# Performance work log

Measured on AMD Instinct MI355X. Metric: run time of the kernel, lower is better.

Reference implementation:

```python
import jax, jax.numpy as jnp
import numpy as np

STRIDE = 2
PADDING = (1, 1)
OUT_PADDING = (0, 0)


def conv_transpose2d(x, weight, bias, stride, padding, out_padding):
    # weight: (Cin, Cout, kh, kw) -- torch ConvTranspose2d layout.
    # The original code does: stride-insert zeros, zero-pad by (k-1), append
    # out_padding rows/cols, valid-conv with the spatially-flipped kernel,
    # then crop `padding` from each side. That is exactly a dilated conv:
    kh, kw = weight.shape[2], weight.shape[3]
    w = jnp.flip(weight, (2, 3)).transpose(1, 0, 2, 3)  # (Cout, Cin, kh, kw)
    pad = ((kh - 1 - padding[0], kh - 1 - padding[0] + out_padding[0]),
           (kw - 1 - padding[1], kw - 1 - padding[1] + out_padding[1]))
    out = jax.lax.conv_general_dilated(
        x, w,
        window_strides=(1, 1),
        padding=pad,
        lhs_dilation=(stride, stride),
        dimension_numbers=('NCHW', 'OIHW', 'NCHW'))
    return out + bias[None, :, None, None]


def setup_inputs() -> dict:
    key = jax.random.key(0)
    k1, k2, k3 = jax.random.split(key, 3)
    Cin, Cout, kh, kw = 256, 128, 4, 4
    bnd = (1.0 / (Cin * kh * kw)) ** 0.5  # matches uniform_(-k**0.5, k**0.5)
    x = jax.random.normal(k1, (16, Cin, 64, 64), dtype=jnp.float32)
    weight = jax.random.uniform(k2, (Cin, Cout, kh, kw), jnp.float32, -bnd, bnd)
    bias = jax.random.uniform(k3, (Cout,), jnp.float32, -bnd, bnd)
    return {"x": x, "weight": weight, "bias": bias}


def reference(x, weight, bias):
    # Output: (16, 128, 128, 128) = (H-1)*2 - 2*1 + 4
    return conv_transpose2d(x, weight, bias, STRIDE, PADDING, OUT_PADDING)
```

## Files before the change

kernel.cpp:

```cpp
#include <hip/hip_runtime.h>
#include <stdint.h>

typedef unsigned short u16;
typedef __bf16 bf16x8 __attribute__((ext_vector_type(8)));
typedef float f32x4 __attribute__((ext_vector_type(4)));
typedef float f32x2 __attribute__((ext_vector_type(2)));

static const size_t XT_BYTES = (size_t)16 * 66 * 66 * 256 * 2;
static const size_t WK_BYTES = (size_t)2 * 2 * 8 * 2 * 2 * 128 * 32 * 2;

__device__ __forceinline__ u16 f2bf(float f) {
  unsigned u = __float_as_uint(f);
  unsigned r = (u + 0x7fff + ((u >> 16) & 1)) >> 16;
  return (u16)r;
}

__device__ __forceinline__ void ld_g2l16(const u16* g, void* l) {
  __builtin_amdgcn_global_load_lds(
      (const __attribute__((address_space(1))) unsigned int*)(uintptr_t)g,
      (__attribute__((address_space(3))) unsigned int*)(unsigned int)(uintptr_t)l,
      16, 0, 0);
}

__device__ __forceinline__ int swz4(int row) { return (row ^ (row >> 2)) & 3; }

__global__ __launch_bounds__(256) void prep_x(const float* __restrict__ x,
                                              u16* __restrict__ xt) {
  __shared__ __align__(16) u16 sh[64 * 264];
  const int t = threadIdx.x;
  const int ihp = blockIdx.x;
  const int n = blockIdx.y;
  u16* xtn = xt + ((size_t)(n * 66 + ihp)) * 66 * 256;
  if (ihp == 0 || ihp == 65) {
    for (int j = 0; j < 9; ++j) {
      int idx = j * 256 + t;
      if (idx < 2112) ((uint4*)xtn)[idx] = make_uint4(0, 0, 0, 0);
    }
    return;
  }
  const int ih = ihp - 1;
  const int iw0 = (t & 15) * 4;
  const int cb = (t >> 4) * 4;
  const int swz = (t & 3) << 3;
  const float* xb = x + (size_t)n * 1048576 + (size_t)ih * 64 + iw0;
#pragma unroll
  for (int it = 0; it < 4; ++it) {
    int ci0 = it * 64 + cb;
    float4 v0 = *(const float4*)(xb + (size_t)(ci0 + 0) * 4096);
    float4 v1 = *(const float4*)(xb + (size_t)(ci0 + 1) * 4096);
    float4 v2 = *(const float4*)(xb + (size_t)(ci0 + 2) * 4096);
    float4 v3 = *(const float4*)(xb + (size_t)(ci0 + 3) * 4096);
    int col = ci0 ^ swz;
    ushort4 u;
    u.x = f2bf(v0.x); u.y = f2bf(v1.x); u.z = f2bf(v2.x); u.w = f2bf(v3.x);
    *(ushort4*)&sh[(iw0 + 0) * 264 + col] = u;
    u.x = f2bf(v0.y); u.y = f2bf(v1.y); u.z = f2bf(v2.y); u.w = f2bf(v3.y);
    *(ushort4*)&sh[(iw0 + 1) * 264 + col] = u;
    u.x = f2bf(v0.z); u.y = f2bf(v1.z); u.z = f2bf(v2.z); u.w = f2bf(v3.z);
    *(ushort4*)&sh[(iw0 + 2) * 264 + col] = u;
    u.x = f2bf(v0.w); u.y = f2bf(v1.w); u.z = f2bf(v2.w); u.w = f2bf(v3.w);
    *(ushort4*)&sh[(iw0 + 3) * 264 + col] = u;
  }
  __syncthreads();
#pragma unroll
  for (int j = 0; j < 8; ++j) {
    int idx = j * 256 + t;
    int iw = idx >> 5;
    int chunk = idx & 31;
    uint4 v = *(const uint4*)&sh[iw * 264 + ((chunk ^ ((iw >> 2) & 3)) << 3)];
    *(uint4*)&xtn[(size_t)(iw + 1) * 256 + chunk * 8] = v;
  }
  if (t < 64) {
    int iwp = (t >> 5) * 65;
    int chunk = t & 31;
    *(uint4*)&xtn[(size_t)iwp * 256 + chunk * 8] = make_uint4(0, 0, 0, 0);
  }
}

__global__ __launch_bounds__(256) void prep_w(const float* __restrict__ w,
                                              u16* __restrict__ wk) {
  int id = blockIdx.x * 256 + threadIdx.x;
  int ci5 = id & 31;
  int co = (id >> 5) & 127;
  int q = (id >> 12) & 1;
  int dw = (id >> 13) & 1;
  int kc = (id >> 14) & 7;
  int dh = (id >> 17) & 1;
  int p = id >> 18;
  int ci = kc * 32 + ci5;
  int kh = 2 * dh + 1 - p;
  int kw = 2 * dw + 1 - q;
  wk[id] = f2bf(w[((ci * 128 + co) * 4 + kh) * 4 + kw]);
}

__global__ __launch_bounds__(256, 2) void gemm_ct(const u16* __restrict__ xt,
                                                  const u16* __restrict__ wk,
                                                  const float* __restrict__ bias,
                                                  float* __restrict__ out) {
  __shared__ __align__(16) u16 As[2][8192];
  __shared__ __align__(16) u16 Bs[2][4224];
  const int t = threadIdx.x;
  const int lane = t & 63;
  const int wv = t >> 6;
  const int wm = wv >> 1, wn = wv & 1;
  const int quad = lane >> 4, l15 = lane & 15;

  const int id = blockIdx.x;
  const int sid = (id & 7) * 128 + (id >> 3);
  const int mt = sid & 31;
  const int n = (sid >> 5) & 15;
  const int p = sid >> 9;
  const int m0 = mt * 2;

  const u16* wkp = wk + (size_t)p * 262144;
  const u16* xtn = xt + (size_t)n * (66 * 66 * 256);

  int aoffs[4];
#pragma unroll
  for (int it = 0; it < 4; ++it) {
    int c = it * 256 + t;
    int co = (c >> 2) & 127;
    aoffs[it] = (c >> 2) * 32 + ((c & 3) ^ swz4(co)) * 8;
  }
  int bsrc[3];
#pragma unroll
  for (int it = 0; it < 3; ++it) {
    int c = it * 256 + t;
    int r = (c >= 264) ? 1 : 0;
    int rem = c - 264 * r;
    int iwp = rem >> 2;
    bsrc[it] = r * 16896 + iwp * 256 + ((rem & 3) ^ swz4(iwp)) * 8;
  }

  int aro[2][4];
#pragma unroll
  for (int q = 0; q < 2; ++q)
#pragma unroll
    for (int i = 0; i < 4; ++i) {
      int co = wm * 64 + i * 16 + l15;
      aro[q][i] = (q * 128 + co) * 32 + (quad ^ swz4(co)) * 8;
    }
  int bro[3][4];
#pragma unroll
  for (int k = 0; k < 3; ++k)
#pragma unroll
    for (int j = 0; j < 4; ++j) {
      int b0 = j * 16 + l15 + k;
      bro[k][j] = wn * 2112 + b0 * 32 + (quad ^ swz4(b0)) * 8;
    }

  f32x4 acc[2][4][4];
#pragma unroll
  for (int q = 0; q < 2; ++q)
#pragma unroll
    for (int i = 0; i < 4; ++i)
#pragma unroll
      for (int j = 0; j < 4; ++j) acc[q][i][j] = (f32x4){0.f, 0.f, 0.f, 0.f};

  const int mpp1 = m0 + p + 1;

  auto stageA = [&](int buf, int s) {
    const u16* asrc = wkp + (size_t)s * 8192;
    u16* Ad = &As[buf][0];
#pragma unroll
    for (int it = 0; it < 4; ++it)
      ld_g2l16(asrc + aoffs[it], Ad + (it * 256 + t) * 8);
  };
  auto stageB = [&](int buf, int pr) {
    const int kc = pr & 7, dh = pr >> 3;
    const u16* bbase = xtn + (size_t)(mpp1 - dh) * 16896 + kc * 32;
    u16* Bd = &Bs[buf][0];
    ld_g2l16(bbase + bsrc[0], Bd + t * 8);
    ld_g2l16(bbase + bsrc[1], Bd + (256 + t) * 8);
    if (t < 16) ld_g2l16(bbase + bsrc[2], Bd + (512 + t) * 8);
  };

  stageA(0, 0);
  stageB(0, 0);
  asm volatile("s_waitcnt vmcnt(0)" ::: "memory");
  __builtin_amdgcn_s_barrier();
  asm volatile("" ::: "memory");

  bf16x8 keep[4];
#pragma unroll 1
  for (int pr = 0; pr < 16; ++pr) {
    const u16* Bc = &Bs[pr & 1][0];
    {
      stageA(1, 2 * pr + 1);
      __builtin_amdgcn_sched_barrier(0);
      if (pr < 15) stageB((pr + 1) & 1, pr + 1);
      __builtin_amdgcn_sched_barrier(0);
      const u16* Ac = &As[0][0];
      bf16x8 a0[4];
#pragma unroll
      for (int i = 0; i < 4; ++i) a0[i] = *(const bf16x8*)(Ac + aro[0][i]);
#pragma unroll
      for (int j = 0; j < 4; ++j) keep[j] = *(const bf16x8*)(Bc + bro[1][j]);
      __builtin_amdgcn_s_setprio(1);
#pragma unroll
      for (int i = 0; i < 4; ++i)
#pragma unroll
        for (int j = 0; j < 4; ++j)
          acc[0][i][j] = __builtin_amdgcn_mfma_f32_16x16x32_bf16(
              a0[i], keep[j], acc[0][i][j], 0, 0, 0);
      __builtin_amdgcn_s_setprio(0);
      bf16x8 a1[4], b2[4];
#pragma unroll
      for (int i = 0; i < 4; ++i) a1[i] = *(const bf16x8*)(Ac + aro[1][i]);
#pragma unroll
      for (int j = 0; j < 4; ++j) b2[j] = *(const bf16x8*)(Bc + bro[2][j]);
      __builtin_amdgcn_s_setprio(1);
#pragma unroll
      for (int i = 0; i < 4; ++i)
#pragma unroll
        for (int j = 0; j < 4; ++j)
          acc[1][i][j] = __builtin_amdgcn_mfma_f32_16x16x32_bf16(
              a1[i], b2[j], acc[1][i][j], 0, 0, 0);
      __builtin_amdgcn_s_setprio(0);
      if (pr < 15) {
        if (wv == 0)
          asm volatile("s_waitcnt lgkmcnt(0) vmcnt(3)" ::: "memory");
        else
          asm volatile("s_waitcnt lgkmcnt(0) vmcnt(2)" ::: "memory");
      } else {
        asm volatile("s_waitcnt lgkmcnt(0) vmcnt(0)" ::: "memory");
      }
      __builtin_amdgcn_s_barrier();
      asm volatile("" ::: "memory");
    }
    {
      if (pr < 15) stageA(0, 2 * pr + 2);
      __builtin_amdgcn_sched_barrier(0);
      const u16* Ac = &As[1][0];
      bf16x8 a0[4], b0[4];
#pragma unroll
      for (int i = 0; i < 4; ++i) a0[i] = *(const bf16x8*)(Ac + aro[0][i]);
#pragma unroll
      for (int j = 0; j < 4; ++j) b0[j] = *(const bf16x8*)(Bc + bro[0][j]);
      __builtin_amdgcn_s_setprio(1);
#pragma unroll
      for (int i = 0; i < 4; ++i)
#pragma unroll
        for (int j = 0; j < 4; ++j)
          acc[0][i][j] = __builtin_amdgcn_mfma_f32_16x16x32_bf16(
              a0[i], b0[j], acc[0][i][j], 0, 0, 0);
      __builtin_amdgcn_s_setprio(0);
      bf16x8 a1[4];
#pragma unroll
      for (int i = 0; i < 4; ++i) a1[i] = *(const bf16x8*)(Ac + aro[1][i]);
      __builtin_amdgcn_s_setprio(1);
#pragma unroll
      for (int i = 0; i < 4; ++i)
#pragma unroll
        for (int j = 0; j < 4; ++j)
          acc[1][i][j] = __builtin_amdgcn_mfma_f32_16x16x32_bf16(
              a1[i], keep[j], acc[1][i][j], 0, 0, 0);
      __builtin_amdgcn_s_setprio(0);
      asm volatile("s_waitcnt lgkmcnt(0) vmcnt(0)" ::: "memory");
      __builtin_amdgcn_s_barrier();
      asm volatile("" ::: "memory");
    }
  }

  const int oh = 2 * (m0 + wn) + p;
#pragma unroll
  for (int i = 0; i < 4; ++i) {
#pragma unroll
    for (int j = 0; j < 4; ++j) {
      int l = j * 16 + l15;
#pragma unroll
      for (int r = 0; r < 4; ++r) {
        int co = wm * 64 + i * 16 + quad * 4 + r;
        float bv = bias[co];
        f32x2 v;
        v.x = acc[0][i][j][r] + bv;
        v.y = acc[1][i][j][r] + bv;
        __builtin_nontemporal_store(
            v, (f32x2*)&out[(((size_t)n * 128 + co) * 128 + oh) * 128 + 2 * l]);
      }
    }
  }
}

__global__ __launch_bounds__(256) void ct_fallback(const float* __restrict__ x,
                                                   const float* __restrict__ w,
                                                   const float* __restrict__ bias,
                                                   float* __restrict__ out) {
  size_t id = (size_t)blockIdx.x * 256 + threadIdx.x;
  if (id >= (size_t)16 * 128 * 128 * 128) return;
  int ow = (int)(id & 127), oh = (int)(id >> 7) & 127;
  int co = (int)(id >> 14) & 127, n = (int)(id >> 21);
  int pp = oh & 1, m = oh >> 1, qq = ow & 1, l = ow >> 1;
  float s = bias[co];
  for (int ci = 0; ci < 256; ++ci) {
    for (int dh = 0; dh < 2; ++dh) {
      int ih = m + pp - dh;
      if (ih < 0 || ih > 63) continue;
      int kh = 2 * dh + 1 - pp;
      for (int dw = 0; dw < 2; ++dw) {
        int iw = l + qq - dw;
        if (iw < 0 || iw > 63) continue;
        int kw = 2 * dw + 1 - qq;
        s += x[(((size_t)n * 256 + ci) * 64 + ih) * 64 + iw] *
             w[((ci * 128 + co) * 4 + kh) * 4 + kw];
      }
    }
  }
  out[id] = s;
}

extern "C" void kernel_launch(void* const* d_in, const int* in_sizes, int n_in,
                              void* d_out, int out_size, void* d_ws, size_t ws_size,
                              hipStream_t stream) {
  const float* x = (const float*)d_in[0];
  const float* w = (const float*)d_in[1];
  const float* bias = (const float*)d_in[2];
  float* out = (float*)d_out;
  if (ws_size >= XT_BYTES + WK_BYTES) {
    u16* xt = (u16*)d_ws;
    u16* wkb = (u16*)((char*)d_ws + XT_BYTES);
    hipLaunchKernelGGL(prep_x, dim3(66, 16), dim3(256), 0, stream, x, xt);
    hipLaunchKernelGGL(prep_w, dim3(2048), dim3(256), 0, stream, w, wkb);
    hipLaunchKernelGGL(gemm_ct, dim3(1024), dim3(256), 0, stream, xt, wkb, bias, out);
  } else {
    hipLaunchKernelGGL(ct_fallback, dim3(131072), dim3(256), 0, stream, x, w, bias, out);
  }
}
```

Baseline: 246.3 us.

## Load weight fragments directly from global to registers and merge prep kernels

The GEMM kernel stops staging the weight (A) tiles through LDS and has each wave load its bf16 weight fragments straight from global memory into registers. The loop is software-pipelined with the A loads interleaved between MFMA groups, and the wait/barrier points are cut from two to one per iteration. The two preprocessing kernels for x and w are merged into one launch, saving a kernel launch. The trade-off is more redundant global/L2 traffic for weights and more register pressure, in exchange for lower LDS use and fewer synchronisations.

```diff
diff --git a/kernel.cpp b/kernel.cpp
--- a/kernel.cpp
+++ b/kernel.cpp
@@ -24,12 +24,30 @@
 
 __device__ __forceinline__ int swz4(int row) { return (row ^ (row >> 2)) & 3; }
 
-__global__ __launch_bounds__(256) void prep_x(const float* __restrict__ x,
-                                              u16* __restrict__ xt) {
+__global__ __launch_bounds__(256) void prep_all(const float* __restrict__ x,
+                                                const float* __restrict__ w,
+                                                u16* __restrict__ xt,
+                                                u16* __restrict__ wk) {
   __shared__ __align__(16) u16 sh[64 * 264];
   const int t = threadIdx.x;
-  const int ihp = blockIdx.x;
-  const int n = blockIdx.y;
+  const int bx = blockIdx.x;
+  if (bx >= 1056) {
+    int id = (bx - 1056) * 256 + t;
+    int ci5 = id & 31;
+    int co = (id >> 5) & 127;
+    int q = (id >> 12) & 1;
+    int dw = (id >> 13) & 1;
+    int kc = (id >> 14) & 7;
+    int dh = (id >> 17) & 1;
+    int p = id >> 18;
+    int ci = kc * 32 + ci5;
+    int kh = 2 * dh + 1 - p;
+    int kw = 2 * dw + 1 - q;
+    wk[id] = f2bf(w[((ci * 128 + co) * 4 + kh) * 4 + kw]);
+    return;
+  }
+  const int n = bx / 66;
+  const int ihp = bx - n * 66;
   u16* xtn = xt + ((size_t)(n * 66 + ihp)) * 66 * 256;
   if (ihp == 0 || ihp == 65) {
     for (int j = 0; j < 9; ++j) {
@@ -77,27 +95,10 @@
   }
 }
 
-__global__ __launch_bounds__(256) void prep_w(const float* __restrict__ w,
-                                              u16* __restrict__ wk) {
-  int id = blockIdx.x * 256 + threadIdx.x;
-  int ci5 = id & 31;
-  int co = (id >> 5) & 127;
-  int q = (id >> 12) & 1;
-  int dw = (id >> 13) & 1;
-  int kc = (id >> 14) & 7;
-  int dh = (id >> 17) & 1;
-  int p = id >> 18;
-  int ci = kc * 32 + ci5;
-  int kh = 2 * dh + 1 - p;
-  int kw = 2 * dw + 1 - q;
-  wk[id] = f2bf(w[((ci * 128 + co) * 4 + kh) * 4 + kw]);
-}
-
 __global__ __launch_bounds__(256, 2) void gemm_ct(const u16* __restrict__ xt,
                                                   const u16* __restrict__ wk,
                                                   const float* __restrict__ bias,
                                                   float* __restrict__ out) {
-  __shared__ __align__(16) u16 As[2][8192];
   __shared__ __align__(16) u16 Bs[2][4224];
   const int t = threadIdx.x;
   const int lane = t & 63;
@@ -112,16 +113,9 @@
   const int p = sid >> 9;
   const int m0 = mt * 2;
 
-  const u16* wkp = wk + (size_t)p * 262144;
+  const u16* wka = wk + (size_t)p * 262144 + wm * 2048 + l15 * 32 + quad * 8;
   const u16* xtn = xt + (size_t)n * (66 * 66 * 256);
 
-  int aoffs[4];
-#pragma unroll
-  for (int it = 0; it < 4; ++it) {
-    int c = it * 256 + t;
-    int co = (c >> 2) & 127;
-    aoffs[it] = (c >> 2) * 32 + ((c & 3) ^ swz4(co)) * 8;
-  }
   int bsrc[3];
 #pragma unroll
   for (int it = 0; it < 3; ++it) {
@@ -132,14 +126,6 @@
     bsrc[it] = r * 16896 + iwp * 256 + ((rem & 3) ^ swz4(iwp)) * 8;
   }
 
-  int aro[2][4];
-#pragma unroll
-  for (int q = 0; q < 2; ++q)
-#pragma unroll
-    for (int i = 0; i < 4; ++i) {
-      int co = wm * 64 + i * 16 + l15;
-      aro[q][i] = (q * 128 + co) * 32 + (quad ^ swz4(co)) * 8;
-    }
   int bro[3][4];
 #pragma unroll
   for (int k = 0; k < 3; ++k)
@@ -159,13 +145,6 @@
 
   const int mpp1 = m0 + p + 1;
 
-  auto stageA = [&](int buf, int s) {
-    const u16* asrc = wkp + (size_t)s * 8192;
-    u16* Ad = &As[buf][0];
-#pragma unroll
-    for (int it = 0; it < 4; ++it)
-      ld_g2l16(asrc + aoffs[it], Ad + (it * 256 + t) * 8);
-  };
   auto stageB = [&](int buf, int pr) {
     const int kc = pr & 7, dh = pr >> 3;
     const u16* bbase = xtn + (size_t)(mpp1 - dh) * 16896 + kc * 32;
@@ -175,7 +154,22 @@
     if (t < 16) ld_g2l16(bbase + bsrc[2], Bd + (512 + t) * 8);
   };
 
-  stageA(0, 0);
+  bf16x8 aC[4], aN[4];
+  auto ldA = [&](bf16x8* a, int s, int q) {
+    const u16* b = wka + (size_t)s * 8192 + q * 4096;
+#pragma unroll
+    for (int i = 0; i < 4; ++i) a[i] = *(const bf16x8*)(b + i * 512);
+  };
+
+#define MFMA16(ACC, AF, BF)                                              \
+  do {                                                                   \
+    _Pragma("unroll") for (int i = 0; i < 4; ++i)                        \
+        _Pragma("unroll") for (int j = 0; j < 4; ++j)                    \
+        ACC[i][j] = __builtin_amdgcn_mfma_f32_16x16x32_bf16(             \
+            AF[i], BF[j], ACC[i][j], 0, 0, 0);                           \
+  } while (0)
+
+  ldA(aC, 0, 0);
   stageB(0, 0);
   asm volatile("s_waitcnt vmcnt(0)" ::: "memory");
   __builtin_amdgcn_s_barrier();
@@ -185,82 +179,47 @@
 #pragma unroll 1
   for (int pr = 0; pr < 16; ++pr) {
     const u16* Bc = &Bs[pr & 1][0];
-    {
-      stageA(1, 2 * pr + 1);
-      __builtin_amdgcn_sched_barrier(0);
-      if (pr < 15) stageB((pr + 1) & 1, pr + 1);
-      __builtin_amdgcn_sched_barrier(0);
-      const u16* Ac = &As[0][0];
-      bf16x8 a0[4];
-#pragma unroll
-      for (int i = 0; i < 4; ++i) a0[i] = *(const bf16x8*)(Ac + aro[0][i]);
-#pragma unroll
-      for (int j = 0; j < 4; ++j) keep[j] = *(const bf16x8*)(Bc + bro[1][j]);
-      __builtin_amdgcn_s_setprio(1);
-#pragma unroll
-      for (int i = 0; i < 4; ++i)
-#pragma unroll
-        for (int j = 0; j < 4; ++j)
-          acc[0][i][j] = __builtin_amdgcn_mfma_f32_16x16x32_bf16(
-              a0[i], keep[j], acc[0][i][j], 0, 0, 0);
-      __builtin_amdgcn_s_setprio(0);
-      bf16x8 a1[4], b2[4];
-#pragma unroll
-      for (int i = 0; i < 4; ++i) a1[i] = *(const bf16x8*)(Ac + aro[1][i]);
-#pragma unroll
-      for (int j = 0; j < 4; ++j) b2[j] = *(const bf16x8*)(Bc + bro[2][j]);
-      __builtin_amdgcn_s_setprio(1);
-#pragma unroll
-      for (int i = 0; i < 4; ++i)
-#pragma unroll
-        for (int j = 0; j < 4; ++j)
-          acc[1][i][j] = __builtin_amdgcn_mfma_f32_16x16x32_bf16(
-              a1[i], b2[j], acc[1][i][j], 0, 0, 0);
-      __builtin_amdgcn_s_setprio(0);
-      if (pr < 15) {
-        if (wv == 0)
-          asm volatile("s_waitcnt lgkmcnt(0) vmcnt(3)" ::: "memory");
-        else
-          asm volatile("s_waitcnt lgkmcnt(0) vmcnt(2)" ::: "memory");
-      } else {
-        asm volatile("s_waitcnt lgkmcnt(0) vmcnt(0)" ::: "memory");
-      }
-      __builtin_amdgcn_s_barrier();
-      asm volatile("" ::: "memory");
-    }
-    {
-      if (pr < 15) stageA(0, 2 * pr + 2);
-      __builtin_amdgcn_sched_barrier(0);
-      const u16* Ac = &As[1][0];
-      bf16x8 a0[4], b0[4];
-#pragma unroll
-      for (int i = 0; i < 4; ++i) a0[i] = *(const bf16x8*)(Ac + aro[0][i]);
-#pragma unroll
-      for (int j = 0; j < 4; ++j) b0[j] = *(const bf16x8*)(Bc + bro[0][j]);
-      __builtin_amdgcn_s_setprio(1);
-#pragma unroll
-      for (int i = 0; i < 4; ++i)
-#pragma unroll
-        for (int j = 0; j < 4; ++j)
-          acc[0][i][j] = __builtin_amdgcn_mfma_f32_16x16x32_bf16(
-              a0[i], b0[j], acc[0][i][j], 0, 0, 0);
-      __builtin_amdgcn_s_setprio(0);
-      bf16x8 a1[4];
-#pragma unroll
-      for (int i = 0; i < 4; ++i) a1[i] = *(const bf16x8*)(Ac + aro[1][i]);
-      __builtin_amdgcn_s_setprio(1);
-#pragma unroll
-      for (int i = 0; i < 4; ++i)
-#pragma unroll
-        for (int j = 0; j < 4; ++j)
-          acc[1][i][j] = __builtin_amdgcn_mfma_f32_16x16x32_bf16(
-              a1[i], keep[j], acc[1][i][j], 0, 0, 0);
-      __builtin_amdgcn_s_setprio(0);
+    const int s0 = 2 * pr;
+    ldA(aN, s0, 1);
+    __builtin_amdgcn_sched_barrier(0);
+    bf16x8 b2[4];
+#pragma unroll
+    for (int j = 0; j < 4; ++j) keep[j] = *(const bf16x8*)(Bc + bro[1][j]);
+#pragma unroll
+    for (int j = 0; j < 4; ++j) b2[j] = *(const bf16x8*)(Bc + bro[2][j]);
+    __builtin_amdgcn_s_setprio(1);
+    MFMA16(acc[0], aC, keep);
+    __builtin_amdgcn_s_setprio(0);
+    __builtin_amdgcn_sched_barrier(0);
+    ldA(aC, s0 + 1, 0);
+    if (pr < 15) stageB((pr + 1) & 1, pr + 1);
+    __builtin_amdgcn_sched_barrier(0);
+    __builtin_amdgcn_s_setprio(1);
+    MFMA16(acc[1], aN, b2);
+    __builtin_amdgcn_s_setprio(0);
+    __builtin_amdgcn_sched_barrier(0);
+    ldA(aN, s0 + 1, 1);
+    __builtin_amdgcn_sched_barrier(0);
+    bf16x8 b0[4];
+#pragma unroll
+    for (int j = 0; j < 4; ++j) b0[j] = *(const bf16x8*)(Bc + bro[0][j]);
+    __builtin_amdgcn_s_setprio(1);
+    MFMA16(acc[0], aC, b0);
+    __builtin_amdgcn_s_setprio(0);
+    __builtin_amdgcn_sched_barrier(0);
+    if (pr < 15) ldA(aC, s0 + 2, 0);
+    __builtin_amdgcn_sched_barrier(0);
+    __builtin_amdgcn_s_setprio(1);
+    MFMA16(acc[1], aN, keep);
+    __builtin_amdgcn_s_setprio(0);
+    if (pr < 15)
+      asm volatile("s_waitcnt lgkmcnt(0) vmcnt(4)" ::: "memory");
+    else
       asm volatile("s_waitcnt lgkmcnt(0) vmcnt(0)" ::: "memory");
-      __builtin_amdgcn_s_barrier();
-      asm volatile("" ::: "memory");
-    }
-  }
+    __builtin_amdgcn_s_barrier();
+    asm volatile("" ::: "memory");
+  }
+#undef MFMA16
 
   const int oh = 2 * (m0 + wn) + p;
 #pragma unroll
@@ -319,8 +278,7 @@
   if (ws_size >= XT_BYTES + WK_BYTES) {
     u16* xt = (u16*)d_ws;
     u16* wkb = (u16*)((char*)d_ws + XT_BYTES);
-    hipLaunchKernelGGL(prep_x, dim3(66, 16), dim3(256), 0, stream, x, xt);
-    hipLaunchKernelGGL(prep_w, dim3(2048), dim3(256), 0, stream, w, wkb);
+    hipLaunchKernelGGL(prep_all, dim3(3104), dim3(256), 0, stream, x, w, xt, wkb);
     hipLaunchKernelGGL(gemm_ct, dim3(1024), dim3(256), 0, stream, xt, wkb, bias, out);
   } else {
     hipLaunchKernelGGL(ct_fallback, dim3(131072), dim3(256), 0, stream, x, w, bias, out);
```

After: 250.8 us. About the same (+1.8%).
